# Kernel optimization log

Hardware: AMD Instinct MI355X
Metric: run time of the kernel (lower is better)

The kernel has to match this reference:

```python
import jax, jax.numpy as jnp
import numpy as np

T = 4194304  # sequence length (2**22)

def setup_inputs() -> dict:
    key = jax.random.key(0)
    k = jax.random.split(key, 7)
    return {
        "x_0": jax.random.normal(k[0], (1, 2), dtype=jnp.float32),
        "u": jax.random.normal(k[1], (2, T), dtype=jnp.float32),
        "timedelta": jax.random.uniform(k[2], (T,), dtype=jnp.float32),
        # scale W_A down so the linear recurrence x_t = A x_{t-1} + ... is stable over 4M steps
        "W_A": 0.3 * jax.random.normal(k[3], (2, 2), dtype=jnp.float32),
        "b_A": 0.1 * jax.random.normal(k[4], (2,), dtype=jnp.float32),
        "W_B": jax.random.normal(k[5], (2, 2), dtype=jnp.float32),
        "b_B": 0.1 * jax.random.normal(k[6], (2,), dtype=jnp.float32),
    }

def reference(x_0, u, timedelta, W_A, b_A, W_B, b_B):
    # forward_PINN: linear state recurrence x_t = A x_{t-1} + B u_t (+biases),
    # output_t = physics_prediction(x_{t-1}, u_t, dt_t) - x_t
    x0 = x_0[0]          # [2] state (x, y)
    u_seq = u.T          # [T, 2] controls (speed, heading)

    def step(x_prev, inp):
        u_t, dt = inp                                  # [2], scalar
        x_t = W_A @ x_prev + b_A + W_B @ u_t + b_B     # [2]
        c = u_t[0] * dt
        pinn = x_prev + jnp.stack([c * jnp.cos(u_t[1]), c * jnp.sin(u_t[1])])
        return x_t, pinn - x_t

    _, x_out = jax.lax.scan(step, x0, (u_seq, timedelta))  # [T, 2]
    return x_out
```

## Files before the change

kernel.cpp:

```cpp
#include <hip/hip_runtime.h>

#define T_TOTAL 4194304
#define S 16
#define NTHREADS 256
#define BLOCK_T (NTHREADS * S)
#define HALO_SEG 4
#define NSEG (NTHREADS + HALO_SEG)

struct M22 { float m00, m01, m10, m11; };
__device__ __forceinline__ M22 mmul(const M22& X, const M22& Y) {
    M22 r;
    r.m00 = fmaf(X.m00, Y.m00, X.m01 * Y.m10);
    r.m01 = fmaf(X.m00, Y.m01, X.m01 * Y.m11);
    r.m10 = fmaf(X.m10, Y.m00, X.m11 * Y.m10);
    r.m11 = fmaf(X.m10, Y.m01, X.m11 * Y.m11);
    return r;
}

struct alignas(16) F16 { float f[16]; };
__device__ __forceinline__ void load16(F16& d, const float* __restrict__ p) {
    const float4* q = (const float4*)p;
    float4 a0 = q[0], a1 = q[1], a2 = q[2], a3 = q[3];
    *(float4*)&d.f[0]  = a0;
    *(float4*)&d.f[4]  = a1;
    *(float4*)&d.f[8]  = a2;
    *(float4*)&d.f[12] = a3;
}

__global__ __launch_bounds__(NTHREADS, 4)
void pinn_rnn_kernel(const float* __restrict__ x0p,
                     const float* __restrict__ u,
                     const float* __restrict__ td,
                     const float* __restrict__ WA,
                     const float* __restrict__ bA,
                     const float* __restrict__ WB,
                     const float* __restrict__ bB,
                     float* __restrict__ out)
{
    __shared__ float2 lc[NSEG];
    __shared__ float2 lout[BLOCK_T];

    const int tid = threadIdx.x;
    const int B0  = blockIdx.x * BLOCK_T;

    const float a00 = WA[0], a01 = WA[1], a10 = WA[2], a11 = WA[3];
    const float w00 = WB[0], w01 = WB[1], w10 = WB[2], w11 = WB[3];
    const float bc0 = bA[0] + bB[0];
    const float bc1 = bA[1] + bB[1];

    const float* u0 = u;
    const float* u1 = u + T_TOTAL;

    const int t0 = B0 + tid * S;
    F16 U0a, U1a, DTa;
    load16(U0a, u0 + t0);
    load16(U1a, u1 + t0);
    load16(DTa, td + t0);

    F16 H0, H1;
    float X0 = 0.f, X1 = 0.f;
    const bool halo_owner = (tid < HALO_SEG);
    if (halo_owner) {
        if (blockIdx.x != 0) {
            const int th = B0 - HALO_SEG * S + tid * S;
            load16(H0, u0 + th);
            load16(H1, u1 + th);
        } else {
            X0 = x0p[0]; X1 = x0p[1];
        }
    }

    M22 A   = { a00, a01, a10, a11 };
    M22 A2  = mmul(A,  A );
    M22 A4  = mmul(A2, A2);
    M22 A8  = mmul(A4, A4);
    M22 M   = mmul(A8, A8);
    M22 Mp2 = mmul(M,  M );
    M22 Mp3 = mmul(Mp2, M);

    {
        float x0v = 0.f, x1v = 0.f;
        #pragma unroll
        for (int j = 0; j < S; ++j) {
            float v0 = fmaf(w00, U0a.f[j], fmaf(w01, U1a.f[j], bc0));
            float v1 = fmaf(w10, U0a.f[j], fmaf(w11, U1a.f[j], bc1));
            float n0 = fmaf(a00, x0v, fmaf(a01, x1v, v0));
            float n1 = fmaf(a10, x0v, fmaf(a11, x1v, v1));
            x0v = n0; x1v = n1;
        }
        lc[tid + HALO_SEG] = make_float2(x0v, x1v);
    }
    if (halo_owner) {
        if (blockIdx.x != 0) {
            float x0v = 0.f, x1v = 0.f;
            #pragma unroll
            for (int j = 0; j < S; ++j) {
                float v0 = fmaf(w00, H0.f[j], fmaf(w01, H1.f[j], bc0));
                float v1 = fmaf(w10, H0.f[j], fmaf(w11, H1.f[j], bc1));
                float n0 = fmaf(a00, x0v, fmaf(a01, x1v, v0));
                float n1 = fmaf(a10, x0v, fmaf(a11, x1v, v1));
                x0v = n0; x1v = n1;
            }
            lc[tid] = make_float2(x0v, x1v);
        } else {
            lc[tid] = make_float2(0.f, 0.f);
        }
    }

    __syncthreads();

    {
        float2 c1 = lc[tid + 3], c2 = lc[tid + 2], c3 = lc[tid + 1], c4 = lc[tid];
        float xi0 = c1.x
                  + fmaf(M.m00,   c2.x, M.m01   * c2.y)
                  + fmaf(Mp2.m00, c3.x, Mp2.m01 * c3.y)
                  + fmaf(Mp3.m00, c4.x, Mp3.m01 * c4.y);
        float xi1 = c1.y
                  + fmaf(M.m10,   c2.x, M.m11   * c2.y)
                  + fmaf(Mp2.m10, c3.x, Mp2.m11 * c3.y)
                  + fmaf(Mp3.m10, c4.x, Mp3.m11 * c4.y);
        if (blockIdx.x == 0 && halo_owner) {
            M22 P;
            if      (tid == 0) P = { 1.f, 0.f, 0.f, 1.f };
            else if (tid == 1) P = M;
            else if (tid == 2) P = Mp2;
            else               P = Mp3;
            xi0 += fmaf(P.m00, X0, P.m01 * X1);
            xi1 += fmaf(P.m10, X0, P.m11 * X1);
        }
        const int xm = tid & 14;
        float2* lrow = lout + tid * S;
        float x0v = xi0, x1v = xi1;
        #pragma unroll
        for (int j = 0; j < S; ++j) {
            float v0 = fmaf(w00, U0a.f[j], fmaf(w01, U1a.f[j], bc0));
            float v1 = fmaf(w10, U0a.f[j], fmaf(w11, U1a.f[j], bc1));
            float n0 = fmaf(a00, x0v, fmaf(a01, x1v, v0));
            float n1 = fmaf(a10, x0v, fmaf(a11, x1v, v1));
            float cc = U0a.f[j] * DTa.f[j];
            float sn, cs;
            __sincosf(U1a.f[j], &sn, &cs);
            lrow[j ^ xm] = make_float2(fmaf(cc, cs, x0v) - n0,
                                       fmaf(cc, sn, x1v) - n1);
            x0v = n0; x1v = n1;
        }
    }
    __syncthreads();

    {
        const float4* lo4 = (const float4*)lout;
        float4* og = (float4*)out + (B0 >> 1);
        #pragma unroll
        for (int m = 0; m < 8; ++m) {
            int f    = m * NTHREADS + tid;
            int i0   = f << 1;
            int slot = i0 ^ ((i0 >> 4) & 14);
            og[f] = lo4[slot >> 1];
        }
    }
}

extern "C" void kernel_launch(void* const* d_in, const int* in_sizes, int n_in,
                              void* d_out, int out_size, void* d_ws, size_t ws_size,
                              hipStream_t stream) {
    const float* x0p = (const float*)d_in[0];
    const float* u   = (const float*)d_in[1];
    const float* td  = (const float*)d_in[2];
    const float* WA  = (const float*)d_in[3];
    const float* bA  = (const float*)d_in[4];
    const float* WB  = (const float*)d_in[5];
    const float* bB  = (const float*)d_in[6];
    float* outp = (float*)d_out;

    dim3 grid(T_TOTAL / BLOCK_T);
    dim3 block(NTHREADS);
    pinn_rnn_kernel<<<grid, block, 0, stream>>>(x0p, u, td, WA, bA, WB, bB, outp);
}
```

Before: 105.4 us.

## Process four windows per block with register prefetch and reused halo

Each block now walks four consecutive 4096-step windows, prefetching the next window's inputs into registers while computing and storing the current one. The halo chunk sums for later windows come from the previous window's last segments kept in shared memory, so the separate halo loads and recomputation are skipped. This cuts redundant halo work and launch/prologue overhead, and overlaps loads with compute. In exchange the grid is four times smaller (256 blocks), there are more barriers per block, register pressure is higher, and launch bounds drop to one block per SM, which may reduce latency hiding.

```diff
diff --git a/kernel.cpp b/kernel.cpp
--- a/kernel.cpp
+++ b/kernel.cpp
@@ -4,6 +4,8 @@
 #define S 16
 #define NTHREADS 256
 #define BLOCK_T (NTHREADS * S)
+#define NWIN 4
+#define NBLOCKS (T_TOTAL / (BLOCK_T * NWIN))
 #define HALO_SEG 4
 #define NSEG (NTHREADS + HALO_SEG)
 
@@ -27,7 +29,7 @@
     *(float4*)&d.f[12] = a3;
 }
 
-__global__ __launch_bounds__(NTHREADS, 4)
+__global__ __launch_bounds__(NTHREADS, 1)
 void pinn_rnn_kernel(const float* __restrict__ x0p,
                      const float* __restrict__ u,
                      const float* __restrict__ td,
@@ -40,8 +42,8 @@
     __shared__ float2 lc[NSEG];
     __shared__ float2 lout[BLOCK_T];
 
-    const int tid = threadIdx.x;
-    const int B0  = blockIdx.x * BLOCK_T;
+    const int tid  = threadIdx.x;
+    const int base = blockIdx.x * (BLOCK_T * NWIN);
 
     const float a00 = WA[0], a01 = WA[1], a10 = WA[2], a11 = WA[3];
     const float w00 = WB[0], w01 = WB[1], w10 = WB[2], w11 = WB[3];
@@ -51,18 +53,20 @@
     const float* u0 = u;
     const float* u1 = u + T_TOTAL;
 
-    const int t0 = B0 + tid * S;
-    F16 U0a, U1a, DTa;
-    load16(U0a, u0 + t0);
-    load16(U1a, u1 + t0);
-    load16(DTa, td + t0);
+    F16 U0c, U1c, DTc;
+    {
+        const int t0 = base + tid * S;
+        load16(U0c, u0 + t0);
+        load16(U1c, u1 + t0);
+        load16(DTc, td + t0);
+    }
 
     F16 H0, H1;
     float X0 = 0.f, X1 = 0.f;
     const bool halo_owner = (tid < HALO_SEG);
     if (halo_owner) {
         if (blockIdx.x != 0) {
-            const int th = B0 - HALO_SEG * S + tid * S;
+            const int th = base - HALO_SEG * S + tid * S;
             load16(H0, u0 + th);
             load16(H1, u1 + th);
         } else {
@@ -82,8 +86,8 @@
         float x0v = 0.f, x1v = 0.f;
         #pragma unroll
         for (int j = 0; j < S; ++j) {
-            float v0 = fmaf(w00, U0a.f[j], fmaf(w01, U1a.f[j], bc0));
-            float v1 = fmaf(w10, U0a.f[j], fmaf(w11, U1a.f[j], bc1));
+            float v0 = fmaf(w00, U0c.f[j], fmaf(w01, U1c.f[j], bc0));
+            float v1 = fmaf(w10, U0c.f[j], fmaf(w11, U1c.f[j], bc1));
             float n0 = fmaf(a00, x0v, fmaf(a01, x1v, v0));
             float n1 = fmaf(a10, x0v, fmaf(a11, x1v, v1));
             x0v = n0; x1v = n1;
@@ -109,53 +113,83 @@
 
     __syncthreads();
 
-    {
-        float2 c1 = lc[tid + 3], c2 = lc[tid + 2], c3 = lc[tid + 1], c4 = lc[tid];
-        float xi0 = c1.x
-                  + fmaf(M.m00,   c2.x, M.m01   * c2.y)
-                  + fmaf(Mp2.m00, c3.x, Mp2.m01 * c3.y)
-                  + fmaf(Mp3.m00, c4.x, Mp3.m01 * c4.y);
-        float xi1 = c1.y
-                  + fmaf(M.m10,   c2.x, M.m11   * c2.y)
-                  + fmaf(Mp2.m10, c3.x, Mp2.m11 * c3.y)
-                  + fmaf(Mp3.m10, c4.x, Mp3.m11 * c4.y);
-        if (blockIdx.x == 0 && halo_owner) {
-            M22 P;
-            if      (tid == 0) P = { 1.f, 0.f, 0.f, 1.f };
-            else if (tid == 1) P = M;
-            else if (tid == 2) P = Mp2;
-            else               P = Mp3;
-            xi0 += fmaf(P.m00, X0, P.m01 * X1);
-            xi1 += fmaf(P.m10, X0, P.m11 * X1);
-        }
-        const int xm = tid & 14;
-        float2* lrow = lout + tid * S;
-        float x0v = xi0, x1v = xi1;
-        #pragma unroll
-        for (int j = 0; j < S; ++j) {
-            float v0 = fmaf(w00, U0a.f[j], fmaf(w01, U1a.f[j], bc0));
-            float v1 = fmaf(w10, U0a.f[j], fmaf(w11, U1a.f[j], bc1));
-            float n0 = fmaf(a00, x0v, fmaf(a01, x1v, v0));
-            float n1 = fmaf(a10, x0v, fmaf(a11, x1v, v1));
-            float cc = U0a.f[j] * DTa.f[j];
-            float sn, cs;
-            __sincosf(U1a.f[j], &sn, &cs);
-            lrow[j ^ xm] = make_float2(fmaf(cc, cs, x0v) - n0,
-                                       fmaf(cc, sn, x1v) - n1);
-            x0v = n0; x1v = n1;
-        }
-    }
-    __syncthreads();
-
-    {
-        const float4* lo4 = (const float4*)lout;
-        float4* og = (float4*)out + (B0 >> 1);
-        #pragma unroll
-        for (int m = 0; m < 8; ++m) {
-            int f    = m * NTHREADS + tid;
-            int i0   = f << 1;
-            int slot = i0 ^ ((i0 >> 4) & 14);
-            og[f] = lo4[slot >> 1];
+    F16 U0n, U1n, DTn;
+
+    for (int w = 0; w < NWIN; ++w) {
+        if (w + 1 < NWIN) {
+            const int tn = base + (w + 1) * BLOCK_T + tid * S;
+            load16(U0n, u0 + tn);
+            load16(U1n, u1 + tn);
+            load16(DTn, td + tn);
+        }
+
+        float2 hc;
+        {
+            float2 c1 = lc[tid + 3], c2 = lc[tid + 2], c3 = lc[tid + 1], c4 = lc[tid];
+            if (halo_owner) hc = lc[NTHREADS + tid];
+            float xi0 = c1.x
+                      + fmaf(M.m00,   c2.x, M.m01   * c2.y)
+                      + fmaf(Mp2.m00, c3.x, Mp2.m01 * c3.y)
+                      + fmaf(Mp3.m00, c4.x, Mp3.m01 * c4.y);
+            float xi1 = c1.y
+                      + fmaf(M.m10,   c2.x, M.m11   * c2.y)
+                      + fmaf(Mp2.m10, c3.x, Mp2.m11 * c3.y)
+                      + fmaf(Mp3.m10, c4.x, Mp3.m11 * c4.y);
+            if (w == 0 && blockIdx.x == 0 && halo_owner) {
+                M22 P;
+                if      (tid == 0) P = { 1.f, 0.f, 0.f, 1.f };
+                else if (tid == 1) P = M;
+                else if (tid == 2) P = Mp2;
+                else               P = Mp3;
+                xi0 += fmaf(P.m00, X0, P.m01 * X1);
+                xi1 += fmaf(P.m10, X0, P.m11 * X1);
+            }
+            const int xm = tid & 14;
+            float2* lrow = lout + tid * S;
+            float x0v = xi0, x1v = xi1;
+            #pragma unroll
+            for (int j = 0; j < S; ++j) {
+                float v0 = fmaf(w00, U0c.f[j], fmaf(w01, U1c.f[j], bc0));
+                float v1 = fmaf(w10, U0c.f[j], fmaf(w11, U1c.f[j], bc1));
+                float n0 = fmaf(a00, x0v, fmaf(a01, x1v, v0));
+                float n1 = fmaf(a10, x0v, fmaf(a11, x1v, v1));
+                float cc = U0c.f[j] * DTc.f[j];
+                float sn, cs;
+                __sincosf(U1c.f[j], &sn, &cs);
+                lrow[j ^ xm] = make_float2(fmaf(cc, cs, x0v) - n0,
+                                           fmaf(cc, sn, x1v) - n1);
+                x0v = n0; x1v = n1;
+            }
+        }
+        __syncthreads();
+
+        {
+            const float4* lo4 = (const float4*)lout;
+            float4* og = (float4*)out + ((base + w * BLOCK_T) >> 1);
+            #pragma unroll
+            for (int m = 0; m < 8; ++m) {
+                int f    = m * NTHREADS + tid;
+                int i0   = f << 1;
+                int slot = i0 ^ ((i0 >> 4) & 14);
+                og[f] = lo4[slot >> 1];
+            }
+        }
+
+        if (w + 1 < NWIN) {
+            float x0v = 0.f, x1v = 0.f;
+            #pragma unroll
+            for (int j = 0; j < S; ++j) {
+                float v0 = fmaf(w00, U0n.f[j], fmaf(w01, U1n.f[j], bc0));
+                float v1 = fmaf(w10, U0n.f[j], fmaf(w11, U1n.f[j], bc1));
+                float n0 = fmaf(a00, x0v, fmaf(a01, x1v, v0));
+                float n1 = fmaf(a10, x0v, fmaf(a11, x1v, v1));
+                x0v = n0; x1v = n1;
+            }
+            lc[tid + HALO_SEG] = make_float2(x0v, x1v);
+            if (halo_owner) lc[tid] = hc;
+
+            U0c = U0n; U1c = U1n; DTc = DTn;
+            __syncthreads();
         }
     }
 }
@@ -172,7 +206,7 @@
     const float* bB  = (const float*)d_in[6];
     float* outp = (float*)d_out;
 
-    dim3 grid(T_TOTAL / BLOCK_T);
+    dim3 grid(NBLOCKS);
     dim3 block(NTHREADS);
     pinn_rnn_kernel<<<grid, block, 0, stream>>>(x0p, u, td, WA, bA, WB, bB, outp);
 }
```

Measured after the change: 109.2 us. 1.04x slower.
